# Kernel tuning notes

Hardware: AMD Instinct MI355X
Metric: run time of the kernel (lower is better)

Reference implementation:

```python
import jax, jax.numpy as jnp
import numpy as np

B = 4096          # number of bags (sequences)
L_AVG = 2048      # average bag length
T = B * L_AVG     # total instances
P = 1 << 20       # param count for L1 penalty
ALPHA = 1e-3
BETA = 0.1
MIN_STD = 1.0
MAX_STD = 1000.0


def setup_inputs() -> dict:
    key = jax.random.key(0)
    k1, k2, k3, k4 = jax.random.split(key, 4)
    # ragged lengths with fixed total T (pairwise perturbation keeps the sum exact)
    rng = np.random.default_rng(0)
    d = rng.integers(-1024, 1025, size=B // 2)
    lengths_np = np.full(B, L_AVG, dtype=np.int64)
    lengths_np[: B // 2] += d
    lengths_np[B // 2 :] -= d
    assert lengths_np.sum() == T and lengths_np.min() >= 1
    seg_ids_np = np.repeat(np.arange(B, dtype=np.int64), lengths_np)
    return {
        "logits": jax.random.normal(k1, (B, 2), dtype=jnp.float32),
        "params": jax.random.normal(k2, (P,), dtype=jnp.float32),
        "attn_weights": jax.random.uniform(k3, (T,), dtype=jnp.float32),
        "labels": jax.random.randint(k4, (B,), 0, 2, dtype=jnp.int64),
        "lengths": jnp.asarray(lengths_np),
        "seg_ids": jnp.asarray(seg_ids_np),
    }


def reference(logits, params, attn_weights, labels, lengths, seg_ids):
    dt = attn_weights.dtype
    n = attn_weights.shape[0]
    seg = lambda v: jax.ops.segment_sum(v, seg_ids, num_segments=B)

    # CrossEntropyLoss (mean reduction)
    logp = jax.nn.log_softmax(logits, axis=-1)
    nll = -jnp.mean(jnp.take_along_axis(logp, labels[:, None], axis=1))

    lengths_f = lengths.astype(dt)
    # position within segment -> x = (pos+1)/len, per-segment arange(1..L)/L
    starts = jnp.cumsum(lengths) - lengths
    pos = jnp.arange(n) - starts[seg_ids]
    x = (pos + 1).astype(dt) / lengths_f[seg_ids]

    y = attn_weights
    sum_y = seg(y)                         # [B]
    mean = seg(x * y) / sum_y              # [B] per-seg attention mean
    ideal_std = jnp.where(labels == 1, MIN_STD, MAX_STD).astype(dt) / lengths_f
    z = (x - mean[seg_ids]) / ideal_std[seg_ids]
    inv_norm = 1.0 / (ideal_std[seg_ids] * jnp.sqrt(2.0 * jnp.pi).astype(dt))
    r_hat = jnp.exp(-0.5 * z * z) * inv_norm
    r = r_hat / (seg(r_hat)[seg_ids] + 1e-6)
    r = jax.lax.stop_gradient(r)           # torch computes r under no_grad

    penalty = (ALPHA / 2) * jnp.sum(jnp.abs(params))
    diff = y - r
    attn_penalty = (BETA / 2) * jnp.mean(seg(diff * diff) / lengths_f)
    loss = nll + penalty + attn_penalty
    return loss, nll
```

## Files before the change

### kernel.cpp

```cpp
#include <hip/hip_runtime.h>


constexpr float INV_SQRT_2PI = 0.39894228040143267794f;


__global__ __launch_bounds__(256) void prep_kernel(
    const float* __restrict__ logits, const float* __restrict__ params,
    const int* __restrict__ labels, const int* __restrict__ lengths,
    int P, int Bn, int nbNll,
    int* __restrict__ starts, float* __restrict__ l1part,
    float* __restrict__ nllpart) {
  __shared__ float s_tmp[4];
  __shared__ int s_wsum[4];
  int bid = blockIdx.x, tid = threadIdx.x;
  int lane = tid & 63, wv = tid >> 6;

  if (bid < 256) {
    const float4* p4 = (const float4*)params;
    int n4 = P >> 2;
    float s = 0.f;
    for (int i = bid * 256 + tid; i < n4; i += 256 * 256) {
      float4 v = p4[i];
      s += fabsf(v.x) + fabsf(v.y) + fabsf(v.z) + fabsf(v.w);
    }
    if (bid == 0 && tid == 0)
      for (int i = n4 << 2; i < P; ++i) s += fabsf(params[i]);
#pragma unroll
    for (int off = 32; off; off >>= 1) s += __shfl_down(s, off, 64);
    if (lane == 0) s_tmp[wv] = s;
    __syncthreads();
    if (tid == 0) l1part[bid] = s_tmp[0] + s_tmp[1] + s_tmp[2] + s_tmp[3];
  } else if (bid < 256 + nbNll) {
    int r = (bid - 256) * 256 + tid;
    float v = 0.f;
    if (r < Bn) {
      float l0 = logits[2 * r], l1 = logits[2 * r + 1];
      float m = fmaxf(l0, l1);
      float lse = m + logf(expf(l0 - m) + expf(l1 - m));
      v = lse - ((labels[r] == 1) ? l1 : l0);
    }
#pragma unroll
    for (int off = 32; off; off >>= 1) v += __shfl_down(v, off, 64);
    if (lane == 0) s_tmp[wv] = v;
    __syncthreads();
    if (tid == 0) nllpart[bid - 256] = s_tmp[0] + s_tmp[1] + s_tmp[2] + s_tmp[3];
  } else {
    int base = tid * 16;
    int lv[16];
    int local = 0;
#pragma unroll
    for (int k = 0; k < 16; ++k) {
      int idx = base + k;
      lv[k] = (idx < Bn) ? lengths[idx] : 0;
      local += lv[k];
    }
    int v = local;
#pragma unroll
    for (int off = 1; off < 64; off <<= 1) {
      int t = __shfl_up(v, off, 64);
      if (lane >= off) v += t;
    }
    if (lane == 63) s_wsum[wv] = v;
    __syncthreads();
    int woff = 0;
    for (int w = 0; w < wv; ++w) woff += s_wsum[w];
    int excl = woff + v - local;
#pragma unroll
    for (int k = 0; k < 16; ++k) {
      int idx = base + k;
      if (idx < Bn) { starts[idx] = excl; excl += lv[k]; }
    }
  }
}

__global__ __launch_bounds__(256) void seg_kernel(
    const float* __restrict__ attn, const int* __restrict__ labels,
    const int* __restrict__ lengths, const int* __restrict__ starts,
    float* __restrict__ segout, int Bn) {
  int wid = (blockIdx.x << 2) + (threadIdx.x >> 6);
  if (wid >= Bn) return;
  int lane = threadIdx.x & 63;
  int L = lengths[wid];
  const float* a = attn + starts[wid];
  float invL = 1.0f / (float)L;

  float sy = 0.f, sxy = 0.f, syy = 0.f;
  for (int i = lane; i < L; i += 64) {
    float y = a[i];
    float x = (float)(i + 1) * invL;
    sy += y;
    sxy = fmaf(x, y, sxy);
    syy = fmaf(y, y, syy);
  }
#pragma unroll
  for (int off = 32; off; off >>= 1) {
    sy  += __shfl_xor(sy, off, 64);
    sxy += __shfl_xor(sxy, off, 64);
  }
  float mean = sxy / sy;
  float ideal_std = ((labels[wid] == 1) ? 1.0f : 1000.0f) * invL;
  float inv_std = 1.0f / ideal_std;
  float inv_norm = INV_SQRT_2PI * inv_std;

  float sr = 0.f, syr = 0.f, srr = 0.f;
  for (int i = lane; i < L; i += 64) {
    float y = a[i];
    float x = (float)(i + 1) * invL;
    float z = (x - mean) * inv_std;
    float rh = expf(-0.5f * z * z) * inv_norm;
    sr  += rh;
    syr = fmaf(y, rh, syr);
    srr = fmaf(rh, rh, srr);
  }
#pragma unroll
  for (int off = 32; off; off >>= 1) {
    syy += __shfl_xor(syy, off, 64);
    sr  += __shfl_xor(sr, off, 64);
    syr += __shfl_xor(syr, off, 64);
    srr += __shfl_xor(srr, off, 64);
  }
  if (lane == 0) {
    float inv_den = 1.0f / (sr + 1e-6f);
    float d2 = syy - 2.0f * syr * inv_den + srr * inv_den * inv_den;
    segout[wid] = d2 * invL;
  }
}

__global__ __launch_bounds__(1024) void finalize_kernel(
    const float* __restrict__ segout, const float* __restrict__ l1part,
    const float* __restrict__ nllpart, float* __restrict__ out, int Bn) {
  __shared__ double s_red[16][3];
  int tid = threadIdx.x, lane = tid & 63, wv = tid >> 6;
  double s_seg = 0.0, s_l1 = 0.0, s_nll = 0.0;
  for (int i = tid; i < Bn; i += 1024) s_seg += (double)segout[i];
  if (tid < 256) s_l1 = (double)l1part[tid];
  if (tid < 16) s_nll = (double)nllpart[tid];
#pragma unroll
  for (int off = 32; off; off >>= 1) {
    s_seg += __shfl_down(s_seg, off, 64);
    s_l1  += __shfl_down(s_l1, off, 64);
    s_nll += __shfl_down(s_nll, off, 64);
  }
  if (lane == 0) { s_red[wv][0] = s_seg; s_red[wv][1] = s_l1; s_red[wv][2] = s_nll; }
  __syncthreads();
  if (tid == 0) {
    double a = 0, b = 0, c = 0;
    for (int w = 0; w < 16; ++w) { a += s_red[w][0]; b += s_red[w][1]; c += s_red[w][2]; }
    double nll = c / (double)Bn;
    double loss = nll + 5e-4 * b + 0.05 * (a / (double)Bn);
    out[0] = (float)loss;
    out[1] = (float)nll;
  }
}

extern "C" void kernel_launch(void* const* d_in, const int* in_sizes, int n_in,
                              void* d_out, int out_size, void* d_ws, size_t ws_size,
                              hipStream_t stream) {
  const float* logits  = (const float*)d_in[0];
  const float* params  = (const float*)d_in[1];
  const float* attn    = (const float*)d_in[2];
  const int*   labels  = (const int*)d_in[3];
  const int*   lengths = (const int*)d_in[4];

  int Bn = in_sizes[3];
  int P  = in_sizes[1];

  int*   starts  = (int*)d_ws;
  float* segout  = (float*)((char*)d_ws + 16384);
  float* l1part  = (float*)((char*)d_ws + 32768);
  float* nllpart = (float*)((char*)d_ws + 33792);

  int nbNll = (Bn + 255) / 256;
  int grid1 = 256 + nbNll + 1;

  hipLaunchKernelGGL(prep_kernel, dim3(grid1), dim3(256), 0, stream,
                     logits, params, labels, lengths, P, Bn, nbNll,
                     starts, l1part, nllpart);
  hipLaunchKernelGGL(seg_kernel, dim3((Bn + 3) / 4), dim3(256), 0, stream,
                     attn, labels, lengths, starts, segout, Bn);
  hipLaunchKernelGGL(finalize_kernel, dim3(1), dim3(1024), 0, stream,
                     segout, l1part, nllpart, (float*)d_out, Bn);
}
```

Before: 140.0 us.

## Fuse prep, segment and finalize kernels into one launch with last-block reduction

```diff
diff --git a/kernel.cpp b/kernel.cpp
--- a/kernel.cpp
+++ b/kernel.cpp
@@ -2,154 +2,190 @@
 
 
 constexpr float INV_SQRT_2PI = 0.39894228040143267794f;
-
-
-__global__ __launch_bounds__(256) void prep_kernel(
+constexpr int L1_BLOCKS = 64;
+
+
+__global__ __launch_bounds__(256) void fused_kernel(
     const float* __restrict__ logits, const float* __restrict__ params,
-    const int* __restrict__ labels, const int* __restrict__ lengths,
-    int P, int Bn, int nbNll,
-    int* __restrict__ starts, float* __restrict__ l1part,
-    float* __restrict__ nllpart) {
-  __shared__ float s_tmp[4];
-  __shared__ int s_wsum[4];
-  int bid = blockIdx.x, tid = threadIdx.x;
-  int lane = tid & 63, wv = tid >> 6;
-
-  if (bid < 256) {
+    const float* __restrict__ attn, const int* __restrict__ labels,
+    const int* __restrict__ lengths, int P, int Bn, int segBlocks,
+    unsigned* __restrict__ counter, double* __restrict__ nllsum,
+    float* __restrict__ l1part, float* __restrict__ segpart,
+    float* __restrict__ out) {
+  const int tid = threadIdx.x, lane = tid & 63, wv = tid >> 6;
+  const int bid = blockIdx.x;
+  __shared__ int s_last;
+  __shared__ double s_redA[4], s_redB[4];
+  __shared__ float s_l1[4];
+
+  if (bid < segBlocks) {
+    int wid = (bid << 2) + wv;
+    if (wid < Bn) {
+      int start = 0;
+      const int4* l4 = (const int4*)lengths;
+      int nq = wid >> 2;
+      for (int q = lane; q < nq; q += 64) {
+        int4 v = l4[q];
+        start += (v.x + v.y) + (v.z + v.w);
+      }
+      if (lane < (wid & 3)) start += lengths[(wid & ~3) + lane];
+#pragma unroll
+      for (int off = 32; off; off >>= 1) start += __shfl_xor(start, off, 64);
+
+      int L = lengths[wid];
+      const float* a = attn + start;
+      float invL = 1.0f / (float)L;
+      int head = (4 - (start & 3)) & 3;
+      if (head > L) head = L;
+      int nb = (L - head) >> 2;
+      int tail = L - head - (nb << 2);
+      const float4* a4 = (const float4*)(a + head);
+
+      float sy = 0.f, sxy = 0.f, syy = 0.f;
+      float yh = 0.f, yt = 0.f;
+      int ih = -1, it = -1;
+      if (lane < head) {
+        ih = lane; yh = a[ih];
+        float x = (float)(ih + 1) * invL;
+        sy += yh; sxy = fmaf(x, yh, sxy); syy = fmaf(yh, yh, syy);
+      }
+      if (lane < tail) {
+        it = head + (nb << 2) + lane; yt = a[it];
+        float x = (float)(it + 1) * invL;
+        sy += yt; sxy = fmaf(x, yt, sxy); syy = fmaf(yt, yt, syy);
+      }
+      float4 yv[12];
+#pragma unroll
+      for (int k = 0; k < 12; ++k) {
+        int q = k * 64 + lane;
+        if (q < nb) {
+          float4 v = a4[q];
+          yv[k] = v;
+          int i0 = head + (q << 2);
+          float x0 = (float)(i0 + 1) * invL;
+          float x1 = (float)(i0 + 2) * invL;
+          float x2 = (float)(i0 + 3) * invL;
+          float x3 = (float)(i0 + 4) * invL;
+          sy += (v.x + v.y) + (v.z + v.w);
+          sxy = fmaf(x0, v.x, fmaf(x1, v.y, fmaf(x2, v.z, fmaf(x3, v.w, sxy))));
+          syy = fmaf(v.x, v.x, fmaf(v.y, v.y, fmaf(v.z, v.z, fmaf(v.w, v.w, syy))));
+        } else {
+          yv[k] = make_float4(0.f, 0.f, 0.f, 0.f);
+        }
+      }
+#pragma unroll
+      for (int off = 32; off; off >>= 1) {
+        sy  += __shfl_xor(sy, off, 64);
+        sxy += __shfl_xor(sxy, off, 64);
+      }
+      float mean = sxy / sy;
+      float inv_std = (labels[wid] == 1) ? (float)L : (float)L * 0.001f;
+      float inv_norm = INV_SQRT_2PI * inv_std;
+
+      float sr = 0.f, syr = 0.f, srr = 0.f;
+      if (ih >= 0) {
+        float z = ((float)(ih + 1) * invL - mean) * inv_std;
+        float r = expf(-0.5f * z * z) * inv_norm;
+        sr += r; syr = fmaf(yh, r, syr); srr = fmaf(r, r, srr);
+      }
+      if (it >= 0) {
+        float z = ((float)(it + 1) * invL - mean) * inv_std;
+        float r = expf(-0.5f * z * z) * inv_norm;
+        sr += r; syr = fmaf(yt, r, syr); srr = fmaf(r, r, srr);
+      }
+#pragma unroll
+      for (int k = 0; k < 12; ++k) {
+        int q = k * 64 + lane;
+        if (q < nb) {
+          int i0 = head + (q << 2);
+          float4 v = yv[k];
+          float z0 = ((float)(i0 + 1) * invL - mean) * inv_std;
+          float z1 = ((float)(i0 + 2) * invL - mean) * inv_std;
+          float z2 = ((float)(i0 + 3) * invL - mean) * inv_std;
+          float z3 = ((float)(i0 + 4) * invL - mean) * inv_std;
+          float r0 = expf(-0.5f * z0 * z0) * inv_norm;
+          float r1 = expf(-0.5f * z1 * z1) * inv_norm;
+          float r2 = expf(-0.5f * z2 * z2) * inv_norm;
+          float r3 = expf(-0.5f * z3 * z3) * inv_norm;
+          sr += (r0 + r1) + (r2 + r3);
+          syr = fmaf(v.x, r0, fmaf(v.y, r1, fmaf(v.z, r2, fmaf(v.w, r3, syr))));
+          srr = fmaf(r0, r0, fmaf(r1, r1, fmaf(r2, r2, fmaf(r3, r3, srr))));
+        }
+      }
+#pragma unroll
+      for (int off = 32; off; off >>= 1) {
+        syy += __shfl_xor(syy, off, 64);
+        sr  += __shfl_xor(sr, off, 64);
+        syr += __shfl_xor(syr, off, 64);
+        srr += __shfl_xor(srr, off, 64);
+      }
+      if (lane == 0) {
+        float inv_den = 1.0f / (sr + 1e-6f);
+        float d2 = syy - 2.0f * syr * inv_den + srr * (inv_den * inv_den);
+        segpart[(bid << 4) + wv] = d2 * invL;
+      }
+    }
+  } else if (bid < segBlocks + L1_BLOCKS) {
+    int b = bid - segBlocks;
     const float4* p4 = (const float4*)params;
     int n4 = P >> 2;
     float s = 0.f;
-    for (int i = bid * 256 + tid; i < n4; i += 256 * 256) {
+    for (int i = (b << 8) + tid; i < n4; i += (L1_BLOCKS << 8)) {
       float4 v = p4[i];
-      s += fabsf(v.x) + fabsf(v.y) + fabsf(v.z) + fabsf(v.w);
-    }
-    if (bid == 0 && tid == 0)
-      for (int i = n4 << 2; i < P; ++i) s += fabsf(params[i]);
+      s += (fabsf(v.x) + fabsf(v.y)) + (fabsf(v.z) + fabsf(v.w));
+    }
+    if (b == 0) {
+      for (int i = (n4 << 2) + tid; i < P; i += 256) s += fabsf(params[i]);
+    }
+#pragma unroll
+    for (int off = 32; off; off >>= 1) s += __shfl_xor(s, off, 64);
+    if (lane == 0) s_l1[wv] = s;
+    __syncthreads();
+    if (tid == 0) l1part[b << 4] = (s_l1[0] + s_l1[1]) + (s_l1[2] + s_l1[3]);
+  } else {
+    double s = 0.0;
+    const float2* lg2 = (const float2*)logits;
+    for (int r = tid; r < Bn; r += 256) {
+      float2 lg = lg2[r];
+      float m = fmaxf(lg.x, lg.y);
+      float lse = m + logf(expf(lg.x - m) + expf(lg.y - m));
+      s += (double)(lse - ((labels[r] == 1) ? lg.y : lg.x));
+    }
 #pragma unroll
     for (int off = 32; off; off >>= 1) s += __shfl_down(s, off, 64);
-    if (lane == 0) s_tmp[wv] = s;
+    if (lane == 0) s_redA[wv] = s;
     __syncthreads();
-    if (tid == 0) l1part[bid] = s_tmp[0] + s_tmp[1] + s_tmp[2] + s_tmp[3];
-  } else if (bid < 256 + nbNll) {
-    int r = (bid - 256) * 256 + tid;
-    float v = 0.f;
-    if (r < Bn) {
-      float l0 = logits[2 * r], l1 = logits[2 * r + 1];
-      float m = fmaxf(l0, l1);
-      float lse = m + logf(expf(l0 - m) + expf(l1 - m));
-      v = lse - ((labels[r] == 1) ? l1 : l0);
-    }
-#pragma unroll
-    for (int off = 32; off; off >>= 1) v += __shfl_down(v, off, 64);
-    if (lane == 0) s_tmp[wv] = v;
-    __syncthreads();
-    if (tid == 0) nllpart[bid - 256] = s_tmp[0] + s_tmp[1] + s_tmp[2] + s_tmp[3];
-  } else {
-    int base = tid * 16;
-    int lv[16];
-    int local = 0;
-#pragma unroll
-    for (int k = 0; k < 16; ++k) {
-      int idx = base + k;
-      lv[k] = (idx < Bn) ? lengths[idx] : 0;
-      local += lv[k];
-    }
-    int v = local;
-#pragma unroll
-    for (int off = 1; off < 64; off <<= 1) {
-      int t = __shfl_up(v, off, 64);
-      if (lane >= off) v += t;
-    }
-    if (lane == 63) s_wsum[wv] = v;
-    __syncthreads();
-    int woff = 0;
-    for (int w = 0; w < wv; ++w) woff += s_wsum[w];
-    int excl = woff + v - local;
-#pragma unroll
-    for (int k = 0; k < 16; ++k) {
-      int idx = base + k;
-      if (idx < Bn) { starts[idx] = excl; excl += lv[k]; }
-    }
+    if (tid == 0) *nllsum = (s_redA[0] + s_redA[1]) + (s_redA[2] + s_redA[3]);
   }
-}
-
-__global__ __launch_bounds__(256) void seg_kernel(
-    const float* __restrict__ attn, const int* __restrict__ labels,
-    const int* __restrict__ lengths, const int* __restrict__ starts,
-    float* __restrict__ segout, int Bn) {
-  int wid = (blockIdx.x << 2) + (threadIdx.x >> 6);
-  if (wid >= Bn) return;
-  int lane = threadIdx.x & 63;
-  int L = lengths[wid];
-  const float* a = attn + starts[wid];
-  float invL = 1.0f / (float)L;
-
-  float sy = 0.f, sxy = 0.f, syy = 0.f;
-  for (int i = lane; i < L; i += 64) {
-    float y = a[i];
-    float x = (float)(i + 1) * invL;
-    sy += y;
-    sxy = fmaf(x, y, sxy);
-    syy = fmaf(y, y, syy);
-  }
-#pragma unroll
-  for (int off = 32; off; off >>= 1) {
-    sy  += __shfl_xor(sy, off, 64);
-    sxy += __shfl_xor(sxy, off, 64);
-  }
-  float mean = sxy / sy;
-  float ideal_std = ((labels[wid] == 1) ? 1.0f : 1000.0f) * invL;
-  float inv_std = 1.0f / ideal_std;
-  float inv_norm = INV_SQRT_2PI * inv_std;
-
-  float sr = 0.f, syr = 0.f, srr = 0.f;
-  for (int i = lane; i < L; i += 64) {
-    float y = a[i];
-    float x = (float)(i + 1) * invL;
-    float z = (x - mean) * inv_std;
-    float rh = expf(-0.5f * z * z) * inv_norm;
-    sr  += rh;
-    syr = fmaf(y, rh, syr);
-    srr = fmaf(rh, rh, srr);
-  }
-#pragma unroll
-  for (int off = 32; off; off >>= 1) {
-    syy += __shfl_xor(syy, off, 64);
-    sr  += __shfl_xor(sr, off, 64);
-    syr += __shfl_xor(syr, off, 64);
-    srr += __shfl_xor(srr, off, 64);
-  }
-  if (lane == 0) {
-    float inv_den = 1.0f / (sr + 1e-6f);
-    float d2 = syy - 2.0f * syr * inv_den + srr * inv_den * inv_den;
-    segout[wid] = d2 * invL;
-  }
-}
-
-__global__ __launch_bounds__(1024) void finalize_kernel(
-    const float* __restrict__ segout, const float* __restrict__ l1part,
-    const float* __restrict__ nllpart, float* __restrict__ out, int Bn) {
-  __shared__ double s_red[16][3];
-  int tid = threadIdx.x, lane = tid & 63, wv = tid >> 6;
-  double s_seg = 0.0, s_l1 = 0.0, s_nll = 0.0;
-  for (int i = tid; i < Bn; i += 1024) s_seg += (double)segout[i];
-  if (tid < 256) s_l1 = (double)l1part[tid];
-  if (tid < 16) s_nll = (double)nllpart[tid];
-#pragma unroll
-  for (int off = 32; off; off >>= 1) {
-    s_seg += __shfl_down(s_seg, off, 64);
-    s_l1  += __shfl_down(s_l1, off, 64);
-    s_nll += __shfl_down(s_nll, off, 64);
-  }
-  if (lane == 0) { s_red[wv][0] = s_seg; s_red[wv][1] = s_l1; s_red[wv][2] = s_nll; }
+
+  __threadfence();
   __syncthreads();
   if (tid == 0) {
-    double a = 0, b = 0, c = 0;
-    for (int w = 0; w < 16; ++w) { a += s_red[w][0]; b += s_red[w][1]; c += s_red[w][2]; }
-    double nll = c / (double)Bn;
-    double loss = nll + 5e-4 * b + 0.05 * (a / (double)Bn);
-    out[0] = (float)loss;
-    out[1] = (float)nll;
+    unsigned old = atomicAdd(counter, 1u);
+    s_last = (old == gridDim.x - 1) ? 1 : 0;
+  }
+  __syncthreads();
+  if (s_last) {
+    __threadfence();
+    double accS = 0.0;
+    for (int j = tid; j < Bn; j += 256)
+      accS += (double)segpart[((j >> 2) << 4) + (j & 3)];
+    double accL = (tid < L1_BLOCKS) ? (double)l1part[tid << 4] : 0.0;
+#pragma unroll
+    for (int off = 32; off; off >>= 1) {
+      accS += __shfl_down(accS, off, 64);
+      accL += __shfl_down(accL, off, 64);
+    }
+    if (lane == 0) { s_redA[wv] = accS; s_redB[wv] = accL; }
+    __syncthreads();
+    if (tid == 0) {
+      double segsum = (s_redA[0] + s_redA[1]) + (s_redA[2] + s_redA[3]);
+      double l1 = (s_redB[0] + s_redB[1]) + (s_redB[2] + s_redB[3]);
+      double nll = *nllsum / (double)Bn;
+      double loss = nll + 5e-4 * l1 + 0.05 * (segsum / (double)Bn);
+      out[0] = (float)loss;
+      out[1] = (float)nll;
+    }
   }
 }
 
@@ -164,20 +200,17 @@
 
   int Bn = in_sizes[3];
   int P  = in_sizes[1];
-
-  int*   starts  = (int*)d_ws;
-  float* segout  = (float*)((char*)d_ws + 16384);
-  float* l1part  = (float*)((char*)d_ws + 32768);
-  float* nllpart = (float*)((char*)d_ws + 33792);
-
-  int nbNll = (Bn + 255) / 256;
-  int grid1 = 256 + nbNll + 1;
-
-  hipLaunchKernelGGL(prep_kernel, dim3(grid1), dim3(256), 0, stream,
-                     logits, params, labels, lengths, P, Bn, nbNll,
-                     starts, l1part, nllpart);
-  hipLaunchKernelGGL(seg_kernel, dim3((Bn + 3) / 4), dim3(256), 0, stream,
-                     attn, labels, lengths, starts, segout, Bn);
-  hipLaunchKernelGGL(finalize_kernel, dim3(1), dim3(1024), 0, stream,
-                     segout, l1part, nllpart, (float*)d_out, Bn);
+  int segBlocks = (Bn + 3) / 4;
+
+  unsigned* counter = (unsigned*)d_ws;
+  double*   nllsum  = (double*)((char*)d_ws + 512);
+  float*    l1part  = (float*)((char*)d_ws + 1024);
+  float*    segpart = (float*)((char*)d_ws + 8192);
+
+  hipMemsetAsync(d_ws, 0, 64, stream);
+
+  int grid = segBlocks + L1_BLOCKS + 1;
+  hipLaunchKernelGGL(fused_kernel, dim3(grid), dim3(256), 0, stream,
+                     logits, params, attn, labels, lengths, P, Bn, segBlocks,
+                     counter, nllsum, l1part, segpart, (float*)d_out);
 }
```

Measured after the change: 224.6 us. 60.5% more time.
